# Optimization experiments

Measured on AMD Instinct MI355X. Metric: run time of the kernel, lower is better.

The kernel has to match this reference:

```python
import jax, jax.numpy as jnp
import numpy as np

IN_F, OUT_F = 4096, 11008
B, S = 2, 4096


def setup_inputs() -> dict:
    key = jax.random.key(0)
    k1, k2, k3, k4 = jax.random.split(key, 4)
    x = jax.random.normal(k1, (B, S, IN_F), dtype=jnp.float32) * 3.0  # pre-smoothed activations
    # int8 weight, stored as int8 (spec'd int32 for harness; math identical)
    weight = jax.random.randint(k2, (OUT_F, IN_F), -127, 128, dtype=jnp.int32).astype(jnp.int8)
    bias = jax.random.normal(k3, (OUT_F,), dtype=jnp.float32)
    dequant_scale = jax.random.uniform(k4, (1,), dtype=jnp.float32) * 0.01 + 0.001  # weight absmax scale
    return {"x": x, "weight": weight, "bias": bias, "dequant_scale": dequant_scale}


def reference(x, weight, bias, dequant_scale):
    x_shape = x.shape
    x2 = x.reshape(-1, x_shape[-1])  # [T, in]
    # per-token activation quantization: absmax -> scale -> round/clamp to int8
    quant_scale = (jnp.max(jnp.abs(x2), axis=-1, keepdims=True) / 127.0).astype(jnp.float32)  # [T,1]
    x_q = jnp.clip(jnp.round(x2 / quant_scale), -128, 127).astype(jnp.int8)
    out_i32 = jnp.matmul(x_q.astype(jnp.int32), weight.astype(jnp.int32).T)  # [T, out]
    # dequant epilogue + bias (all fp32)
    dscale = dequant_scale.reshape(()) * quant_scale  # [T,1]
    out = dscale * out_i32.astype(jnp.float32) + bias
    return out.reshape(*x_shape[:-1], -1).astype(x.dtype)
```

## Files before the change

### kernel.cpp

```cpp
#include <hip/hip_runtime.h>

#define T_TOKENS 8192
#define IN_F 4096
#define OUT_F 11008

#define BM 256
#define BN 256
#define BK 64
#define NT (IN_F / BK)

typedef __attribute__((ext_vector_type(4))) int v4i;
typedef __attribute__((ext_vector_type(16))) int v16i;

__device__ __forceinline__ void load_lds16(const signed char* g, const signed char* l) {
    __builtin_amdgcn_global_load_lds(
        (const __attribute__((address_space(1))) void*)g,
        (__attribute__((address_space(3))) void*)l, 16, 0, 0);
}

__global__ __launch_bounds__(256) void quant_kernel(
        const float* __restrict__ x, signed char* __restrict__ xq,
        float* __restrict__ qscale) {
    const int row = blockIdx.x;
    const float4* xr = (const float4*)(x + (size_t)row * IN_F);
    float4 v[4];
    float am = 0.f;
#pragma unroll
    for (int i = 0; i < 4; ++i) {
        v[i] = xr[threadIdx.x + i * 256];
        am = fmaxf(am, fmaxf(fmaxf(fabsf(v[i].x), fabsf(v[i].y)),
                             fmaxf(fabsf(v[i].z), fabsf(v[i].w))));
    }
#pragma unroll
    for (int off = 32; off > 0; off >>= 1)
        am = fmaxf(am, __shfl_xor(am, off, 64));
    __shared__ float wmax[4];
    const int wid = threadIdx.x >> 6;
    if ((threadIdx.x & 63) == 0) wmax[wid] = am;
    __syncthreads();
    float amax = fmaxf(fmaxf(wmax[0], wmax[1]), fmaxf(wmax[2], wmax[3]));
    float qs = amax * (1.0f / 127.0f);
    if (qs < 1e-30f) qs = 1e-30f;
    const float inv = 1.0f / qs;
    if (threadIdx.x == 0) qscale[row] = qs;
    int* xqo = (int*)(xq + (size_t)row * IN_F);
#pragma unroll
    for (int i = 0; i < 4; ++i) {
        int q0 = (int)rintf(v[i].x * inv);
        int q1 = (int)rintf(v[i].y * inv);
        int q2 = (int)rintf(v[i].z * inv);
        int q3 = (int)rintf(v[i].w * inv);
        q0 = max(-128, min(127, q0));
        q1 = max(-128, min(127, q1));
        q2 = max(-128, min(127, q2));
        q3 = max(-128, min(127, q3));
        unsigned p = (unsigned)(q0 & 255) | ((unsigned)(q1 & 255) << 8) |
                     ((unsigned)(q2 & 255) << 16) | ((unsigned)(q3 & 255) << 24);
        xqo[threadIdx.x + i * 256] = (int)p;
    }
}

__global__ __launch_bounds__(256) void repack_kernel(
        const int* __restrict__ w32, signed char* __restrict__ w8, int n4) {
    int idx = blockIdx.x * 256 + threadIdx.x;
    const int stride = gridDim.x * 256;
    for (int i = idx; i < n4; i += stride) {
        v4i w = ((const v4i*)w32)[i];
        unsigned p = (unsigned)(w[0] & 255) | ((unsigned)(w[1] & 255) << 8) |
                     ((unsigned)(w[2] & 255) << 16) | ((unsigned)(w[3] & 255) << 24);
        ((int*)w8)[i] = (int)p;
    }
}

__global__ __launch_bounds__(512, 2) void gemm_kernel(
        const signed char* __restrict__ A, const signed char* __restrict__ B,
        const float* __restrict__ qscale, const float* __restrict__ bias,
        const float* __restrict__ dqs, float* __restrict__ out) {
    __shared__ __align__(16) signed char smem[3 * 32768];

    const int tid = threadIdx.x;
    const int wid = tid >> 6;
    const int lane = tid & 63;
    const int wm = wid >> 2;
    const int wn = wid & 3;
    const int l31 = lane & 31;
    const int hi = lane >> 5;

    const int wg = ((int)blockIdx.x & 7) * 172 + ((int)blockIdx.x >> 3);
    const int m0 = (wg & 31) * BM;
    const int n0 = (wg >> 5) * BN;

    const signed char* aSrc[2];
    const signed char* bSrc[2];
    int ldsDst[2];
#pragma unroll
    for (int c = 0; c < 2; ++c) {
        const int L = c * 8192 + tid * 16;
        const int row = L >> 6;
        const int slot = (L >> 4) & 3;
        const int col = ((slot ^ ((row >> 1) & 3)) << 4);
        aSrc[c] = A + (size_t)(m0 + row) * IN_F + col;
        bSrc[c] = B + (size_t)(n0 + row) * IN_F + col;
        ldsDst[c] = c * 8192 + wid * 1024;
    }
    auto STAGE = [&](int bufBase, int koff) {
#pragma unroll
        for (int c = 0; c < 2; ++c)
            load_lds16(aSrc[c] + koff, smem + bufBase + ldsDst[c]);
#pragma unroll
        for (int c = 0; c < 2; ++c)
            load_lds16(bSrc[c] + koff, smem + bufBase + 16384 + ldsDst[c]);
    };

    int aOff[4][2], bOff[2][2];
#pragma unroll
    for (int im = 0; im < 4; ++im) {
        const int r = wm * 128 + im * 32 + l31;
#pragma unroll
        for (int ks = 0; ks < 2; ++ks) {
            const int c16 = ks * 2 + hi;
            aOff[im][ks] = r * 64 + ((c16 ^ ((r >> 1) & 3)) << 4);
        }
    }
#pragma unroll
    for (int in = 0; in < 2; ++in) {
        const int r = wn * 64 + in * 32 + l31;
#pragma unroll
        for (int ks = 0; ks < 2; ++ks) {
            const int c16 = ks * 2 + hi;
            bOff[in][ks] = 16384 + r * 64 + ((c16 ^ ((r >> 1) & 3)) << 4);
        }
    }

    v16i acc[4][2] = {};

    int bb0 = 0, bb1 = 32768, bb2 = 65536;
    STAGE(bb0, 0);
    STAGE(bb1, BK);

    for (int t = 0; t < NT; ++t) {
        if (t + 1 < NT) {
            asm volatile("s_waitcnt vmcnt(4)" ::: "memory");
        } else {
            asm volatile("s_waitcnt vmcnt(0)" ::: "memory");
        }
        __builtin_amdgcn_sched_barrier(0);
        __builtin_amdgcn_s_barrier();
        __builtin_amdgcn_sched_barrier(0);

        if (t + 2 < NT) STAGE(bb2, (t + 2) * BK);

#pragma unroll
        for (int ks = 0; ks < 2; ++ks) {
            v4i a[4], b[2];
#pragma unroll
            for (int im = 0; im < 4; ++im)
                a[im] = *(const v4i*)(smem + bb0 + aOff[im][ks]);
#pragma unroll
            for (int in = 0; in < 2; ++in)
                b[in] = *(const v4i*)(smem + bb0 + bOff[in][ks]);
            __builtin_amdgcn_s_setprio(1);
#pragma unroll
            for (int im = 0; im < 4; ++im)
#pragma unroll
                for (int in = 0; in < 2; ++in)
                    acc[im][in] = __builtin_amdgcn_mfma_i32_32x32x32_i8(
                        a[im], b[in], acc[im][in], 0, 0, 0);
            __builtin_amdgcn_s_setprio(0);
        }
        const int tmp = bb0; bb0 = bb1; bb1 = bb2; bb2 = tmp;
    }

    const float dq = dqs[0];
#pragma unroll
    for (int im = 0; im < 4; ++im) {
        float qsv[16];
#pragma unroll
        for (int r = 0; r < 16; ++r) {
            const int trow = wm * 128 + im * 32 + (r & 3) + 8 * (r >> 2) + 4 * hi;
            qsv[r] = dq * qscale[m0 + trow];
        }
#pragma unroll
        for (int in = 0; in < 2; ++in) {
            const int col = n0 + wn * 64 + in * 32 + l31;
            const float bv = bias[col];
#pragma unroll
            for (int r = 0; r < 16; ++r) {
                const int trow = wm * 128 + im * 32 + (r & 3) + 8 * (r >> 2) + 4 * hi;
                out[(size_t)(m0 + trow) * OUT_F + col] =
                    qsv[r] * (float)acc[im][in][r] + bv;
            }
        }
    }
}

extern "C" void kernel_launch(void* const* d_in, const int* in_sizes, int n_in,
                              void* d_out, int out_size, void* d_ws, size_t ws_size,
                              hipStream_t stream) {
    const float* x    = (const float*)d_in[0];
    const int*   w32  = (const int*)d_in[1];
    const float* bias = (const float*)d_in[2];
    const float* dqs  = (const float*)d_in[3];
    float* out = (float*)d_out;

    signed char* xq = (signed char*)d_ws;
    float* qscale   = (float*)((char*)d_ws + (size_t)T_TOKENS * IN_F);
    signed char* w8 = (signed char*)((char*)d_ws + (size_t)T_TOKENS * IN_F
                                     + (size_t)T_TOKENS * 4);

    quant_kernel<<<T_TOKENS, 256, 0, stream>>>(x, xq, qscale);
    repack_kernel<<<2048, 256, 0, stream>>>(w32, w8, OUT_F * IN_F / 4);
    dim3 g((T_TOKENS / BM) * (OUT_F / BN));
    gemm_kernel<<<g, 512, 0, stream>>>(xq, w8, qscale, bias, dqs, out);
}
```

Before: 557.6 us.

## Split GEMM main loop into four ping-pong phases interleaving LDS reads, loads, MFMAs

The K-loop body is restructured into four phases. Each phase issues a subset of LDS fragment reads plus one global-to-LDS prefetch chunk, then runs a group of four MFMAs, with workgroup barriers between phases. This spreads memory traffic across the MFMA stream so loads and LDS reads overlap compute better. The workgroup-to-tile mapping is also changed so each XCD gets a contiguous group of M tiles, aiming at better L2 reuse. The extra barriers per iteration add sync overhead, and the vmcnt bookkeeping is now more delicate.

Result: faster. 535.5 us (-4.0%).

```diff
diff --git a/kernel.cpp b/kernel.cpp
--- a/kernel.cpp
+++ b/kernel.cpp
@@ -86,31 +86,29 @@
     const int l31 = lane & 31;
     const int hi = lane >> 5;
 
-    const int wg = ((int)blockIdx.x & 7) * 172 + ((int)blockIdx.x >> 3);
-    const int m0 = (wg & 31) * BM;
-    const int n0 = (wg >> 5) * BN;
-
-    const signed char* aSrc[2];
-    const signed char* bSrc[2];
-    int ldsDst[2];
-#pragma unroll
-    for (int c = 0; c < 2; ++c) {
-        const int L = c * 8192 + tid * 16;
+    const int b = (int)blockIdx.x;
+    const int xcd = b & 7;
+    const int idx = b >> 3;
+    const int m0 = (xcd * 4 + (idx & 3)) * BM;
+    const int n0 = (idx >> 2) * BN;
+
+    const signed char* gSrc[4];
+    int ldsOff[4];
+#pragma unroll
+    for (int c = 0; c < 4; ++c) {
+        const int cc = c & 1;
+        const int L = cc * 8192 + tid * 16;
         const int row = L >> 6;
         const int slot = (L >> 4) & 3;
         const int col = ((slot ^ ((row >> 1) & 3)) << 4);
-        aSrc[c] = A + (size_t)(m0 + row) * IN_F + col;
-        bSrc[c] = B + (size_t)(n0 + row) * IN_F + col;
-        ldsDst[c] = c * 8192 + wid * 1024;
-    }
-    auto STAGE = [&](int bufBase, int koff) {
-#pragma unroll
-        for (int c = 0; c < 2; ++c)
-            load_lds16(aSrc[c] + koff, smem + bufBase + ldsDst[c]);
-#pragma unroll
-        for (int c = 0; c < 2; ++c)
-            load_lds16(bSrc[c] + koff, smem + bufBase + 16384 + ldsDst[c]);
-    };
+        if (c < 2) {
+            gSrc[c] = A + (size_t)(m0 + row) * IN_F + col;
+            ldsOff[c] = cc * 8192 + wid * 1024;
+        } else {
+            gSrc[c] = B + (size_t)(n0 + row) * IN_F + col;
+            ldsOff[c] = 16384 + cc * 8192 + wid * 1024;
+        }
+    }
 
     int aOff[4][2], bOff[2][2];
 #pragma unroll
@@ -118,8 +116,8 @@
         const int r = wm * 128 + im * 32 + l31;
 #pragma unroll
         for (int ks = 0; ks < 2; ++ks) {
-            const int c16 = ks * 2 + hi;
-            aOff[im][ks] = r * 64 + ((c16 ^ ((r >> 1) & 3)) << 4);
+            const int slot = ks * 2 + hi;
+            aOff[im][ks] = r * 64 + ((slot ^ ((r >> 1) & 3)) << 4);
         }
     }
 #pragma unroll
@@ -127,47 +125,111 @@
         const int r = wn * 64 + in * 32 + l31;
 #pragma unroll
         for (int ks = 0; ks < 2; ++ks) {
-            const int c16 = ks * 2 + hi;
-            bOff[in][ks] = 16384 + r * 64 + ((c16 ^ ((r >> 1) & 3)) << 4);
+            const int slot = ks * 2 + hi;
+            bOff[in][ks] = 16384 + r * 64 + ((slot ^ ((r >> 1) & 3)) << 4);
         }
     }
 
     v16i acc[4][2] = {};
 
     int bb0 = 0, bb1 = 32768, bb2 = 65536;
-    STAGE(bb0, 0);
-    STAGE(bb1, BK);
+#pragma unroll
+    for (int c = 0; c < 4; ++c) load_lds16(gSrc[c], smem + bb0 + ldsOff[c]);
+#pragma unroll
+    for (int c = 0; c < 4; ++c) load_lds16(gSrc[c] + BK, smem + bb1 + ldsOff[c]);
+    asm volatile("s_waitcnt vmcnt(4)" ::: "memory");
+    __builtin_amdgcn_sched_barrier(0);
+    __builtin_amdgcn_s_barrier();
 
     for (int t = 0; t < NT; ++t) {
-        if (t + 1 < NT) {
+        const int koff2 = (t + 2) * BK;
+        const bool stage = (t + 2 < NT);
+        v4i a01[2][2], a23[2][2], b0[2], b1[2];
+
+#pragma unroll
+        for (int im = 0; im < 2; ++im)
+#pragma unroll
+            for (int ks = 0; ks < 2; ++ks)
+                a01[im][ks] = *(const v4i*)(smem + bb0 + aOff[im][ks]);
+#pragma unroll
+        for (int ks = 0; ks < 2; ++ks)
+            b0[ks] = *(const v4i*)(smem + bb0 + bOff[0][ks]);
+        if (stage) load_lds16(gSrc[0] + koff2, smem + bb2 + ldsOff[0]);
+        __builtin_amdgcn_sched_barrier(0);
+        __builtin_amdgcn_s_barrier();
+        asm volatile("s_waitcnt lgkmcnt(0)" ::: "memory");
+        __builtin_amdgcn_sched_barrier(0);
+        __builtin_amdgcn_s_setprio(1);
+#pragma unroll
+        for (int ks = 0; ks < 2; ++ks)
+#pragma unroll
+            for (int im = 0; im < 2; ++im)
+                acc[im][0] = __builtin_amdgcn_mfma_i32_32x32x32_i8(
+                    a01[im][ks], b0[ks], acc[im][0], 0, 0, 0);
+        __builtin_amdgcn_s_setprio(0);
+        __builtin_amdgcn_sched_barrier(0);
+        __builtin_amdgcn_s_barrier();
+
+#pragma unroll
+        for (int ks = 0; ks < 2; ++ks)
+            b1[ks] = *(const v4i*)(smem + bb0 + bOff[1][ks]);
+        if (stage) load_lds16(gSrc[1] + koff2, smem + bb2 + ldsOff[1]);
+        __builtin_amdgcn_sched_barrier(0);
+        __builtin_amdgcn_s_barrier();
+        asm volatile("s_waitcnt lgkmcnt(0)" ::: "memory");
+        __builtin_amdgcn_sched_barrier(0);
+        __builtin_amdgcn_s_setprio(1);
+#pragma unroll
+        for (int ks = 0; ks < 2; ++ks)
+#pragma unroll
+            for (int im = 0; im < 2; ++im)
+                acc[im][1] = __builtin_amdgcn_mfma_i32_32x32x32_i8(
+                    a01[im][ks], b1[ks], acc[im][1], 0, 0, 0);
+        __builtin_amdgcn_s_setprio(0);
+        __builtin_amdgcn_sched_barrier(0);
+        __builtin_amdgcn_s_barrier();
+
+#pragma unroll
+        for (int im = 0; im < 2; ++im)
+#pragma unroll
+            for (int ks = 0; ks < 2; ++ks)
+                a23[im][ks] = *(const v4i*)(smem + bb0 + aOff[2 + im][ks]);
+        if (stage) load_lds16(gSrc[2] + koff2, smem + bb2 + ldsOff[2]);
+        __builtin_amdgcn_sched_barrier(0);
+        __builtin_amdgcn_s_barrier();
+        asm volatile("s_waitcnt lgkmcnt(0)" ::: "memory");
+        __builtin_amdgcn_sched_barrier(0);
+        __builtin_amdgcn_s_setprio(1);
+#pragma unroll
+        for (int ks = 0; ks < 2; ++ks)
+#pragma unroll
+            for (int im = 0; im < 2; ++im)
+                acc[2 + im][1] = __builtin_amdgcn_mfma_i32_32x32x32_i8(
+                    a23[im][ks], b1[ks], acc[2 + im][1], 0, 0, 0);
+        __builtin_amdgcn_s_setprio(0);
+        __builtin_amdgcn_sched_barrier(0);
+        __builtin_amdgcn_s_barrier();
+
+        if (stage) load_lds16(gSrc[3] + koff2, smem + bb2 + ldsOff[3]);
+        __builtin_amdgcn_sched_barrier(0);
+        __builtin_amdgcn_s_barrier();
+        __builtin_amdgcn_s_setprio(1);
+#pragma unroll
+        for (int ks = 0; ks < 2; ++ks)
+#pragma unroll
+            for (int im = 0; im < 2; ++im)
+                acc[2 + im][0] = __builtin_amdgcn_mfma_i32_32x32x32_i8(
+                    a23[im][ks], b0[ks], acc[2 + im][0], 0, 0, 0);
+        __builtin_amdgcn_s_setprio(0);
+        __builtin_amdgcn_sched_barrier(0);
+        if (t < NT - 2) {
             asm volatile("s_waitcnt vmcnt(4)" ::: "memory");
         } else {
             asm volatile("s_waitcnt vmcnt(0)" ::: "memory");
         }
         __builtin_amdgcn_sched_barrier(0);
         __builtin_amdgcn_s_barrier();
-        __builtin_amdgcn_sched_barrier(0);
-
-        if (t + 2 < NT) STAGE(bb2, (t + 2) * BK);
-
-#pragma unroll
-        for (int ks = 0; ks < 2; ++ks) {
-            v4i a[4], b[2];
-#pragma unroll
-            for (int im = 0; im < 4; ++im)
-                a[im] = *(const v4i*)(smem + bb0 + aOff[im][ks]);
-#pragma unroll
-            for (int in = 0; in < 2; ++in)
-                b[in] = *(const v4i*)(smem + bb0 + bOff[in][ks]);
-            __builtin_amdgcn_s_setprio(1);
-#pragma unroll
-            for (int im = 0; im < 4; ++im)
-#pragma unroll
-                for (int in = 0; in < 2; ++in)
-                    acc[im][in] = __builtin_amdgcn_mfma_i32_32x32x32_i8(
-                        a[im], b[in], acc[im][in], 0, 0, 0);
-            __builtin_amdgcn_s_setprio(0);
-        }
+
         const int tmp = bb0; bb0 = bb1; bb1 = bb2; bb2 = tmp;
     }
 
```
